# Performance work log

Hardware: AMD Instinct MI355X
Metric: run time of the kernel (lower is better)

The kernel has to match this reference:

```python
import jax, jax.numpy as jnp
import numpy as np

DIM = 256
N_EMBED = 8192
BETA = 0.25


def setup_inputs() -> dict:
    key = jax.random.key(0)
    k1, k2, k3, k4 = jax.random.split(key, 4)
    inp = {
        "input": jax.random.normal(k1, (16, 1024, DIM), dtype=jnp.float32),
        # nn.Embedding weight init: normal(0, dim**-0.5)
        "embed_weight": jax.random.normal(k2, (N_EMBED, DIM), dtype=jnp.float32) * (DIM ** -0.5),
        # nn.Linear(dim, dim): weight [out, in], bias [out]
        "proj_w": jax.random.normal(k3, (DIM, DIM), dtype=jnp.float32) * (DIM ** -0.5),
        "proj_b": jax.random.normal(k4, (DIM,), dtype=jnp.float32) * 0.01,
    }
    return inp


def reference(input, embed_weight, proj_w, proj_b):
    flatten = input.reshape(-1, DIM)                      # [N, d]
    # projected codebook: Linear(embedding.weight)
    quant_codebook = embed_weight @ proj_w.T + proj_b     # [K, d]
    d = (jnp.sum(flatten ** 2, axis=1, keepdims=True)
         + jnp.sum(quant_codebook ** 2, axis=1)
         - 2.0 * jnp.einsum('nd,kd->nk', flatten, quant_codebook))  # [N, K]
    min_encoding_indices = jnp.argmin(d, axis=1)          # [N]
    z_quantize = quant_codebook[min_encoding_indices].reshape(input.shape)
    sg = jax.lax.stop_gradient
    diff = jnp.mean((sg(z_quantize) - input) ** 2)
    commit_loss = jnp.mean((z_quantize - sg(input)) ** 2)
    diff = diff + BETA * commit_loss                      # legacy=True branch
    # straight-through estimator
    z_quantize = input + sg(z_quantize - input)
    return (z_quantize, diff, min_encoding_indices)
```

## Files before the change

kernel.cpp:

```cpp
#include <hip/hip_runtime.h>

#define DIMD   256
#define NTOK   16384
#define NCODE  8192
#define NELEM  (NTOK * DIMD)

#define BM 128
#define BK 128
#define BD 32
#define PAD 4
#define LDS_STRIDE (BM + PAD)

#define CODES_PER_BLOCK 1024
#define TOK_PER_BLOCK   256
#define NGROUPS (CODES_PER_BLOCK / 16)
#define MARGIN 0.5f
#define EBUF_CAP 1024

#define PROJ_BLOCKS ((NCODE / BM) * (DIMD / BK))
#define CONV_BLOCKS (NTOK / 4)

typedef float floatx4 __attribute__((ext_vector_type(4)));
typedef short short8  __attribute__((ext_vector_type(8)));
typedef unsigned int u32;

__device__ __forceinline__ unsigned short f2bf(float f) {
    unsigned u = __float_as_uint(f);
    unsigned r = (u + 0x7FFFu + ((u >> 16) & 1u)) >> 16;
    return (unsigned short)r;
}

__device__ __forceinline__ void gl_lds16(const void* g, void* l) {
    __builtin_amdgcn_global_load_lds(
        (const __attribute__((address_space(1))) u32*)g,
        (__attribute__((address_space(3))) u32*)l, 16, 0, 0);
}

__device__ __forceinline__ unsigned fkey(float f) {
    unsigned u = __float_as_uint(f);
    return (u & 0x80000000u) ? ~u : (u | 0x80000000u);
}
__device__ __forceinline__ float funkey(unsigned k) {
    unsigned u = (k & 0x80000000u) ? (k & 0x7FFFFFFFu) : ~k;
    return __uint_as_float(u);
}

__device__ __forceinline__ size_t cb2_idx(int row, int col) {
    return ((size_t)((row >> 4) * 8 + (col >> 5))) * 512
         + (size_t)((((col >> 3) & 3) * 16 + (row & 15)) * 8 + (col & 7));
}

__global__ __launch_bounds__(256, 3)
void prep_kernel(const float* __restrict__ E, const float* __restrict__ W,
                 const float* __restrict__ bias, float* __restrict__ C,
                 unsigned short* __restrict__ Cb2,
                 float* __restrict__ cnormA, float* __restrict__ cnormB,
                 const float* __restrict__ X, float* __restrict__ xnorm,
                 unsigned short* __restrict__ Xb,
                 unsigned long long* __restrict__ fin,
                 unsigned* __restrict__ minkey,
                 unsigned* __restrict__ cnt, float* __restrict__ out)
{
    __shared__ float smem[2 * BD * LDS_STRIDE];

    const int bid = blockIdx.x;
    const int tid = threadIdx.x;

    if (bid >= PROJ_BLOCKS) {
        const int row0 = (bid - PROJ_BLOCKS) * 4;
        const int wave = tid >> 6;
        const int lane = tid & 63;
        const int row  = row0 + wave;
        float4 v = *(const float4*)&X[(size_t)row * DIMD + lane * 4];
        ushort4 h = {f2bf(v.x), f2bf(v.y), f2bf(v.z), f2bf(v.w)};
        *(ushort4*)&Xb[(size_t)row * DIMD + lane * 4] = h;
        float s = v.x * v.x + v.y * v.y + v.z * v.z + v.w * v.w;
#pragma unroll
        for (int off = 1; off < 64; off <<= 1) s += __shfl_xor(s, off);
        if (lane == 0) xnorm[row] = s;
        if (tid < 4) {
            fin[row0 + tid]    = ~0ull;
            minkey[row0 + tid] = ~0u;
        }
        if (bid == PROJ_BLOCKS && tid == 0) { *cnt = 0; out[NELEM] = 0.f; }
        return;
    }

    float* As = smem;
    float* Bs = smem + BD * LDS_STRIDE;

    const int tx  = tid & 15;
    const int ty  = tid >> 4;
    const int m0  = (bid & 63) * BM;
    const int j0  = (bid >> 6) * BK;

    const int srow = tid >> 3;
    const int scol = (tid & 7) * 4;

    float acc[8][8];
#pragma unroll
    for (int i = 0; i < 8; ++i)
#pragma unroll
        for (int j = 0; j < 8; ++j) acc[i][j] = 0.f;

    for (int dc = 0; dc < DIMD / BD; ++dc) {
        const int d0 = dc * BD;
        __syncthreads();
#pragma unroll
        for (int rr = 0; rr < 4; ++rr) {
            const int r = srow + rr * 32;
            float4 av = *(const float4*)&E[(size_t)(m0 + r) * DIMD + d0 + scol];
            As[(scol + 0) * LDS_STRIDE + r] = av.x;
            As[(scol + 1) * LDS_STRIDE + r] = av.y;
            As[(scol + 2) * LDS_STRIDE + r] = av.z;
            As[(scol + 3) * LDS_STRIDE + r] = av.w;
            float4 bv = *(const float4*)&W[(size_t)(j0 + r) * DIMD + d0 + scol];
            Bs[(scol + 0) * LDS_STRIDE + r] = bv.x;
            Bs[(scol + 1) * LDS_STRIDE + r] = bv.y;
            Bs[(scol + 2) * LDS_STRIDE + r] = bv.z;
            Bs[(scol + 3) * LDS_STRIDE + r] = bv.w;
        }
        __syncthreads();
#pragma unroll 4
        for (int d = 0; d < BD; ++d) {
            float4 a0 = *(float4*)&As[d * LDS_STRIDE + ty * 4];
            float4 a1 = *(float4*)&As[d * LDS_STRIDE + 64 + ty * 4];
            float4 b0 = *(float4*)&Bs[d * LDS_STRIDE + tx * 4];
            float4 b1 = *(float4*)&Bs[d * LDS_STRIDE + 64 + tx * 4];
            float a[8] = {a0.x, a0.y, a0.z, a0.w, a1.x, a1.y, a1.z, a1.w};
            float b[8] = {b0.x, b0.y, b0.z, b0.w, b1.x, b1.y, b1.z, b1.w};
#pragma unroll
            for (int i = 0; i < 8; ++i)
#pragma unroll
                for (int j = 0; j < 8; ++j) acc[i][j] = fmaf(a[i], b[j], acc[i][j]);
        }
    }

    __syncthreads();
    float* red = smem;

    float4 bja = *(const float4*)&bias[j0 + tx * 4];
    float4 bjb = *(const float4*)&bias[j0 + 64 + tx * 4];
#pragma unroll
    for (int i = 0; i < 8; ++i) {
        const int mloc = (i < 4) ? (ty * 4 + i) : (64 + ty * 4 + (i - 4));
        const int row  = m0 + mloc;
        const size_t rbase = (size_t)row * DIMD;
        float o[8] = {acc[i][0] + bja.x, acc[i][1] + bja.y, acc[i][2] + bja.z, acc[i][3] + bja.w,
                      acc[i][4] + bjb.x, acc[i][5] + bjb.y, acc[i][6] + bjb.z, acc[i][7] + bjb.w};
        *(float4*)&C[rbase + j0 + tx * 4]      = *(float4*)&o[0];
        *(float4*)&C[rbase + j0 + 64 + tx * 4] = *(float4*)&o[4];
        ushort4 h0 = {f2bf(o[0]), f2bf(o[1]), f2bf(o[2]), f2bf(o[3])};
        ushort4 h1 = {f2bf(o[4]), f2bf(o[5]), f2bf(o[6]), f2bf(o[7])};
        *(ushort4*)&Cb2[cb2_idx(row, j0 + tx * 4)]      = h0;
        *(ushort4*)&Cb2[cb2_idx(row, j0 + 64 + tx * 4)] = h1;
        float p = 0.f;
#pragma unroll
        for (int j = 0; j < 8; ++j) p = fmaf(o[j], o[j], p);
        red[mloc * 16 + tx] = p;
    }
    __syncthreads();
    if (tid < 128) {
        float s = 0.f;
#pragma unroll
        for (int k = 0; k < 16; ++k) s += red[tid * 16 + k];
        float* dst = (j0 == 0) ? cnormA : cnormB;
        dst[m0 + tid] = s;
    }
}

__global__ __launch_bounds__(256, 2)
void dist_min_kernel(const unsigned short* __restrict__ Xb,
                     const unsigned short* __restrict__ Cb2,
                     const float* __restrict__ cnormA,
                     const float* __restrict__ cnormB,
                     unsigned* __restrict__ minkey)
{
    __shared__ short Bls[2][4096];
    __shared__ float cnl[CODES_PER_BLOCK];

    const int tid  = threadIdx.x;
    const int lane = tid & 63;
    const int wv   = tid >> 6;
    const int l15  = lane & 15;
    const int quad = lane >> 4;
    const int tok0 = blockIdx.x * TOK_PER_BLOCK + wv * 64;
    const int cbase = blockIdx.y * CODES_PER_BLOCK;

    {
        const int t4 = tid * 4;
        float4 va = *(const float4*)&cnormA[cbase + t4];
        float4 vb = *(const float4*)&cnormB[cbase + t4];
        cnl[t4 + 0] = va.x + vb.x;
        cnl[t4 + 1] = va.y + vb.y;
        cnl[t4 + 2] = va.z + vb.z;
        cnl[t4 + 3] = va.w + vb.w;
    }

    const unsigned short* bsrc = Cb2 + (size_t)cbase * DIMD;
    auto STAGE = [&](int g) {
        const unsigned short* s = bsrc + (size_t)g * 4096 + wv * 1024 + lane * 8;
        short* d = &Bls[g & 1][wv * 1024];
        gl_lds16(s,       d);
        gl_lds16(s + 512, d + 512);
    };
    STAGE(0);
    STAGE(1);

    short8 a[4][8];
#pragma unroll
    for (int i = 0; i < 4; ++i) {
        const unsigned short* ap = Xb + (size_t)(tok0 + i * 16 + l15) * DIMD + quad * 8;
#pragma unroll
        for (int ks = 0; ks < 8; ++ks)
            a[i][ks] = *(const short8*)(ap + ks * 32);
    }

    float runv[16];
#pragma unroll
    for (int s = 0; s < 16; ++s) runv[s] = 3.4e38f;

    __syncthreads();

    for (int g = 0; g < NGROUPS; ++g) {
        const short* bp = &Bls[g & 1][lane * 8];
        short8 bc[8];
#pragma unroll
        for (int ks = 0; ks < 8; ++ks) bc[ks] = *(const short8*)(bp + ks * 512);
        const float cnc = cnl[g * 16 + l15];

        floatx4 acc[4];
#pragma unroll
        for (int i = 0; i < 4; ++i) acc[i] = (floatx4){0.f, 0.f, 0.f, 0.f};
#pragma unroll
        for (int ks = 0; ks < 8; ++ks)
#pragma unroll
            for (int i = 0; i < 4; ++i)
                acc[i] = __builtin_amdgcn_mfma_f32_16x16x32_bf16(a[i][ks], bc[ks], acc[i], 0, 0, 0);

#pragma unroll
        for (int i = 0; i < 4; ++i)
#pragma unroll
            for (int r = 0; r < 4; ++r)
                runv[i * 4 + r] = fminf(runv[i * 4 + r], fmaf(-2.f, acc[i][r], cnc));

        __syncthreads();
        if (g + 2 < NGROUPS) STAGE(g + 2);
    }

#pragma unroll
    for (int s = 0; s < 16; ++s) {
        float m = runv[s];
#pragma unroll
        for (int off = 1; off < 16; off <<= 1) m = fminf(m, __shfl_xor(m, off));
        runv[s] = m;
    }
    if (l15 == 0) {
#pragma unroll
        for (int i = 0; i < 4; ++i)
#pragma unroll
            for (int r = 0; r < 4; ++r)
                atomicMin(&minkey[tok0 + i * 16 + quad * 4 + r], fkey(runv[i * 4 + r]));
    }
}

__global__ __launch_bounds__(256, 2)
void dist_emit_kernel(const unsigned short* __restrict__ Xb,
                      const unsigned short* __restrict__ Cb2,
                      const float* __restrict__ cnormA,
                      const float* __restrict__ cnormB,
                      const unsigned* __restrict__ minkey,
                      unsigned* __restrict__ list, unsigned* __restrict__ count,
                      unsigned cap)
{
    __shared__ short Bls[2][4096];
    __shared__ float cnl[CODES_PER_BLOCK];
    __shared__ float tokthr[TOK_PER_BLOCK];
    __shared__ unsigned ebuf[EBUF_CAP];
    __shared__ unsigned ecnt, gbase;

    const int tid  = threadIdx.x;
    const int lane = tid & 63;
    const int wv   = tid >> 6;
    const int l15  = lane & 15;
    const int quad = lane >> 4;
    const int tok0b = blockIdx.x * TOK_PER_BLOCK;
    const int tok0 = tok0b + wv * 64;
    const int cbase = blockIdx.y * CODES_PER_BLOCK;

    {
        const int t4 = tid * 4;
        float4 va = *(const float4*)&cnormA[cbase + t4];
        float4 vb = *(const float4*)&cnormB[cbase + t4];
        cnl[t4 + 0] = va.x + vb.x;
        cnl[t4 + 1] = va.y + vb.y;
        cnl[t4 + 2] = va.z + vb.z;
        cnl[t4 + 3] = va.w + vb.w;
    }
    tokthr[tid] = funkey(minkey[tok0b + tid]) + MARGIN;
    if (tid == 0) ecnt = 0;

    const unsigned short* bsrc = Cb2 + (size_t)cbase * DIMD;
    auto STAGE = [&](int g) {
        const unsigned short* s = bsrc + (size_t)g * 4096 + wv * 1024 + lane * 8;
        short* d = &Bls[g & 1][wv * 1024];
        gl_lds16(s,       d);
        gl_lds16(s + 512, d + 512);
    };
    STAGE(0);
    STAGE(1);

    short8 a[4][8];
#pragma unroll
    for (int i = 0; i < 4; ++i) {
        const unsigned short* ap = Xb + (size_t)(tok0 + i * 16 + l15) * DIMD + quad * 8;
#pragma unroll
        for (int ks = 0; ks < 8; ++ks)
            a[i][ks] = *(const short8*)(ap + ks * 32);
    }

    __syncthreads();

    float thr[16];
#pragma unroll
    for (int i = 0; i < 4; ++i)
#pragma unroll
        for (int r = 0; r < 4; ++r)
            thr[i * 4 + r] = tokthr[wv * 64 + i * 16 + quad * 4 + r];

    for (int g = 0; g < NGROUPS; ++g) {
        const int code0 = cbase + g * 16;
        const short* bp = &Bls[g & 1][lane * 8];
        short8 bc[8];
#pragma unroll
        for (int ks = 0; ks < 8; ++ks) bc[ks] = *(const short8*)(bp + ks * 512);
        const float cnc = cnl[g * 16 + l15];

        floatx4 acc[4];
#pragma unroll
        for (int i = 0; i < 4; ++i) acc[i] = (floatx4){0.f, 0.f, 0.f, 0.f};
#pragma unroll
        for (int ks = 0; ks < 8; ++ks)
#pragma unroll
            for (int i = 0; i < 4; ++i)
                acc[i] = __builtin_amdgcn_mfma_f32_16x16x32_bf16(a[i][ks], bc[ks], acc[i], 0, 0, 0);

        unsigned mask = 0;
#pragma unroll
        for (int i = 0; i < 4; ++i)
#pragma unroll
            for (int r = 0; r < 4; ++r) {
                const float dd = fmaf(-2.f, acc[i][r], cnc);
                if (dd < thr[i * 4 + r]) mask |= (1u << (i * 4 + r));
            }

        if (__any(mask != 0)) {
            if (mask) {
                unsigned pos = atomicAdd(&ecnt, (unsigned)__popc(mask));
#pragma unroll
                for (int i = 0; i < 4; ++i)
#pragma unroll
                    for (int r = 0; r < 4; ++r) {
                        const int s = i * 4 + r;
                        if (mask & (1u << s)) {
                            const unsigned token = tok0 + i * 16 + quad * 4 + r;
                            const unsigned entry = (token << 13) | (unsigned)(code0 + l15);
                            if (pos < EBUF_CAP) ebuf[pos] = entry;
                            else { unsigned gp = atomicAdd(count, 1u); if (gp < cap) list[gp] = entry; }
                            ++pos;
                        }
                    }
            }
        }

        __syncthreads();
        if (g + 2 < NGROUPS) STAGE(g + 2);
    }

    __syncthreads();
    const unsigned n = (ecnt < EBUF_CAP) ? ecnt : EBUF_CAP;
    if (tid == 0) gbase = atomicAdd(count, n);
    __syncthreads();
    const unsigned gb = gbase;
    for (unsigned i = tid; i < n; i += 256) {
        const unsigned p = gb + i;
        if (p < cap) list[p] = ebuf[i];
    }
}

__global__ __launch_bounds__(256)
void rescore_kernel(const float* __restrict__ X, const float* __restrict__ C,
                    const float* __restrict__ xnorm,
                    const float* __restrict__ cnormA,
                    const float* __restrict__ cnormB,
                    const unsigned* __restrict__ list, const unsigned* __restrict__ count,
                    unsigned cap, unsigned long long* __restrict__ fin)
{
    const int lane = threadIdx.x & 63;
    const int g16  = lane & 15;
    const int sub  = lane >> 4;
    const int gid  = ((blockIdx.x * 256 + threadIdx.x) >> 6) * 4 + sub;
    const int ng   = ((gridDim.x * 256) >> 6) * 4;
    unsigned n = *count; if (n > cap) n = cap;

    for (unsigned c = gid; c < n; c += ng) {
        const unsigned e = list[c];
        const unsigned tok = e >> 13, code = e & 8191u;
        const float* xr = &X[(size_t)tok * DIMD];
        const float* cr = &C[(size_t)code * DIMD];
        float dot = 0.f;
#pragma unroll
        for (int r = 0; r < 4; ++r) {
            float4 x4 = *(const float4*)&xr[r * 64 + g16 * 4];
            float4 c4 = *(const float4*)&cr[r * 64 + g16 * 4];
            dot = fmaf(x4.x, c4.x, dot);
            dot = fmaf(x4.y, c4.y, dot);
            dot = fmaf(x4.z, c4.z, dot);
            dot = fmaf(x4.w, c4.w, dot);
        }
#pragma unroll
        for (int d = 1; d < 16; d <<= 1) dot += __shfl_xor(dot, d);
        if (g16 == 0) {
            const float dd = xnorm[tok] + (cnormA[code] + cnormB[code]) - 2.f * dot;
            const unsigned long long p =
                ((unsigned long long)__float_as_uint(dd) << 32) | code;
            atomicMin(&fin[tok], p);
        }
    }
}

__global__ __launch_bounds__(256)
void finalize_kernel(const float* __restrict__ X, const float* __restrict__ C,
                     const unsigned long long* __restrict__ fin,
                     float* __restrict__ out)
{
    __shared__ float part[4];
    const int lane = threadIdx.x & 63;
    const int wv   = threadIdx.x >> 6;
    const int t0   = blockIdx.x * 64;

    float local = 0.f;
    for (int it = 0; it < 16; ++it) {
        const int t = t0 + wv * 16 + it;
        const unsigned code = (unsigned)(fin[t] & 0xFFFFFFFFull);
        float4 c4 = *(const float4*)&C[(size_t)code * DIMD + lane * 4];
        float4 x4 = *(const float4*)&X[(size_t)t * DIMD + lane * 4];
        float4 w  = {c4.x - x4.x, c4.y - x4.y, c4.z - x4.z, c4.w - x4.w};
        local += w.x * w.x + w.y * w.y + w.z * w.z + w.w * w.w;
        float4 zq = {x4.x + w.x, x4.y + w.y, x4.z + w.z, x4.w + w.w};
        *(float4*)&out[(size_t)t * DIMD + lane * 4] = zq;
        if (lane == 0) out[NELEM + 1 + t] = (float)code;
    }
#pragma unroll
    for (int off = 1; off < 64; off <<= 1) local += __shfl_xor(local, off);
    if (lane == 0) part[wv] = local;
    __syncthreads();
    if (threadIdx.x == 0) {
        const float s = part[0] + part[1] + part[2] + part[3];
        atomicAdd(&out[NELEM], s * (1.25f / (float)NELEM));
    }
}

extern "C" void kernel_launch(void* const* d_in, const int* in_sizes, int n_in,
                              void* d_out, int out_size, void* d_ws, size_t ws_size,
                              hipStream_t stream)
{
    const float* X = (const float*)d_in[0];
    const float* E = (const float*)d_in[1];
    const float* W = (const float*)d_in[2];
    const float* b = (const float*)d_in[3];
    float* out = (float*)d_out;

    char* w = (char*)d_ws;
    float* C            = (float*)w;           w += (size_t)NCODE * DIMD * 4;
    unsigned short* Xb  = (unsigned short*)w;  w += (size_t)NTOK * DIMD * 2;
    unsigned short* Cb2 = (unsigned short*)w;  w += (size_t)NCODE * DIMD * 2;
    float* xnorm        = (float*)w;           w += (size_t)NTOK * 4;
    float* cnormA       = (float*)w;           w += (size_t)NCODE * 4;
    float* cnormB       = (float*)w;           w += (size_t)NCODE * 4;
    unsigned* cnt       = (unsigned*)w;        w += 256;
    unsigned long long* fin = (unsigned long long*)w; w += (size_t)NTOK * 8;
    unsigned* minkey    = (unsigned*)w;        w += (size_t)NTOK * 4;
    unsigned* list      = (unsigned*)w;

    size_t used = (size_t)(w - (char*)d_ws);
    size_t avail = (ws_size > used) ? (ws_size - used) / 4 : 0;
    unsigned cap = (unsigned)((avail > 16777216u) ? 16777216u : avail);

    prep_kernel<<<PROJ_BLOCKS + CONV_BLOCKS, 256, 0, stream>>>(
        E, W, b, C, Cb2, cnormA, cnormB, X, xnorm, Xb, fin, minkey, cnt, out);
    dist_min_kernel<<<dim3(NTOK / TOK_PER_BLOCK, NCODE / CODES_PER_BLOCK), 256, 0, stream>>>(
        Xb, Cb2, cnormA, cnormB, minkey);
    dist_emit_kernel<<<dim3(NTOK / TOK_PER_BLOCK, NCODE / CODES_PER_BLOCK), 256, 0, stream>>>(
        Xb, Cb2, cnormA, cnormB, minkey, list, cnt, cap);
    rescore_kernel<<<1024, 256, 0, stream>>>(X, C, xnorm, cnormA, cnormB, list, cnt, cap, fin);
    finalize_kernel<<<NTOK / 64, 256, 0, stream>>>(X, C, fin, out);
}
```

Measured before the change: 273.7 us.

## Restructure emit kernel: share token tile across waves, stream codes via registers

```diff
diff --git a/kernel.cpp b/kernel.cpp
--- a/kernel.cpp
+++ b/kernel.cpp
@@ -11,11 +11,15 @@
 #define PAD 4
 #define LDS_STRIDE (BM + PAD)
 
+#define MARGIN 0.5f
+#define EBUF_CAP 1024
+
 #define CODES_PER_BLOCK 1024
 #define TOK_PER_BLOCK   256
-#define NGROUPS (CODES_PER_BLOCK / 16)
-#define MARGIN 0.5f
-#define EBUF_CAP 1024
+#define MIN_NGROUPS (CODES_PER_BLOCK / 16)
+#define EM_SPLITS 4
+#define EM_CPW (NCODE / EM_SPLITS / 4)
+#define EM_NGROUPS (EM_CPW / 16)
 
 #define PROJ_BLOCKS ((NCODE / BM) * (DIMD / BK))
 #define CONV_BLOCKS (NTOK / 4)
@@ -222,7 +226,7 @@
 
     __syncthreads();
 
-    for (int g = 0; g < NGROUPS; ++g) {
+    for (int g = 0; g < MIN_NGROUPS; ++g) {
         const short* bp = &Bls[g & 1][lane * 8];
         short8 bc[8];
 #pragma unroll
@@ -245,7 +249,7 @@
                 runv[i * 4 + r] = fminf(runv[i * 4 + r], fmaf(-2.f, acc[i][r], cnc));
 
         __syncthreads();
-        if (g + 2 < NGROUPS) STAGE(g + 2);
+        if (g + 2 < MIN_NGROUPS) STAGE(g + 2);
     }
 
 #pragma unroll
@@ -273,9 +277,7 @@
                       unsigned* __restrict__ list, unsigned* __restrict__ count,
                       unsigned cap)
 {
-    __shared__ short Bls[2][4096];
-    __shared__ float cnl[CODES_PER_BLOCK];
-    __shared__ float tokthr[TOK_PER_BLOCK];
+    __shared__ float tokthr[64];
     __shared__ unsigned ebuf[EBUF_CAP];
     __shared__ unsigned ecnt, gbase;
 
@@ -284,31 +286,12 @@
     const int wv   = tid >> 6;
     const int l15  = lane & 15;
     const int quad = lane >> 4;
-    const int tok0b = blockIdx.x * TOK_PER_BLOCK;
-    const int tok0 = tok0b + wv * 64;
-    const int cbase = blockIdx.y * CODES_PER_BLOCK;
-
-    {
-        const int t4 = tid * 4;
-        float4 va = *(const float4*)&cnormA[cbase + t4];
-        float4 vb = *(const float4*)&cnormB[cbase + t4];
-        cnl[t4 + 0] = va.x + vb.x;
-        cnl[t4 + 1] = va.y + vb.y;
-        cnl[t4 + 2] = va.z + vb.z;
-        cnl[t4 + 3] = va.w + vb.w;
-    }
-    tokthr[tid] = funkey(minkey[tok0b + tid]) + MARGIN;
+    const int tok0 = blockIdx.x * 64;
+    const int cbase = blockIdx.y * (NCODE / EM_SPLITS) + wv * EM_CPW;
+
     if (tid == 0) ecnt = 0;
-
-    const unsigned short* bsrc = Cb2 + (size_t)cbase * DIMD;
-    auto STAGE = [&](int g) {
-        const unsigned short* s = bsrc + (size_t)g * 4096 + wv * 1024 + lane * 8;
-        short* d = &Bls[g & 1][wv * 1024];
-        gl_lds16(s,       d);
-        gl_lds16(s + 512, d + 512);
-    };
-    STAGE(0);
-    STAGE(1);
+    if (tid < 64) tokthr[tid] = funkey(minkey[tok0 + tid]) + MARGIN;
+    __syncthreads();
 
     short8 a[4][8];
 #pragma unroll
@@ -319,22 +302,31 @@
             a[i][ks] = *(const short8*)(ap + ks * 32);
     }
 
-    __syncthreads();
-
     float thr[16];
 #pragma unroll
     for (int i = 0; i < 4; ++i)
 #pragma unroll
         for (int r = 0; r < 4; ++r)
-            thr[i * 4 + r] = tokthr[wv * 64 + i * 16 + quad * 4 + r];
-
-    for (int g = 0; g < NGROUPS; ++g) {
+            thr[i * 4 + r] = tokthr[i * 16 + quad * 4 + r];
+
+    const unsigned short* bp0 = Cb2 + (size_t)cbase * DIMD + lane * 8;
+
+    short8 breg[2][8];
+    float  cnr[2];
+#pragma unroll
+    for (int ks = 0; ks < 8; ++ks) breg[0][ks] = *(const short8*)(bp0 + ks * 512);
+    cnr[0] = cnormA[cbase + l15] + cnormB[cbase + l15];
+
+    auto group_body = [&](int g, short8 (&bc)[8], short8 (&bn)[8],
+                          float cnc, float& cnn) {
         const int code0 = cbase + g * 16;
-        const short* bp = &Bls[g & 1][lane * 8];
-        short8 bc[8];
-#pragma unroll
-        for (int ks = 0; ks < 8; ++ks) bc[ks] = *(const short8*)(bp + ks * 512);
-        const float cnc = cnl[g * 16 + l15];
+        if (g + 1 < EM_NGROUPS) {
+            const unsigned short* bpn = bp0 + (size_t)(g + 1) * 4096;
+#pragma unroll
+            for (int ks = 0; ks < 8; ++ks) bn[ks] = *(const short8*)(bpn + ks * 512);
+            const int cnx = code0 + 16 + l15;
+            cnn = cnormA[cnx] + cnormB[cnx];
+        }
 
         floatx4 acc[4];
 #pragma unroll
@@ -372,9 +364,11 @@
                     }
             }
         }
-
-        __syncthreads();
-        if (g + 2 < NGROUPS) STAGE(g + 2);
+    };
+
+    for (int gg = 0; gg < EM_NGROUPS; gg += 2) {
+        group_body(gg,     breg[0], breg[1], cnr[0], cnr[1]);
+        group_body(gg + 1, breg[1], breg[0], cnr[1], cnr[0]);
     }
 
     __syncthreads();
@@ -491,7 +485,7 @@
         E, W, b, C, Cb2, cnormA, cnormB, X, xnorm, Xb, fin, minkey, cnt, out);
     dist_min_kernel<<<dim3(NTOK / TOK_PER_BLOCK, NCODE / CODES_PER_BLOCK), 256, 0, stream>>>(
         Xb, Cb2, cnormA, cnormB, minkey);
-    dist_emit_kernel<<<dim3(NTOK / TOK_PER_BLOCK, NCODE / CODES_PER_BLOCK), 256, 0, stream>>>(
+    dist_emit_kernel<<<dim3(NTOK / 64, EM_SPLITS), 256, 0, stream>>>(
         Xb, Cb2, cnormA, cnormB, minkey, list, cnt, cap);
     rescore_kernel<<<1024, 256, 0, stream>>>(X, C, xnorm, cnormA, cnormB, list, cnt, cap, fin);
     finalize_kernel<<<NTOK / 64, 256, 0, stream>>>(X, C, fin, out);
```

New measurement: 273.2 us. About the same (-0.2%).
